# Kernel tuning notes

Hardware: AMD Instinct MI355X
Metric: run time of the kernel (lower is better)

## Reference

```python
import math
import jax, jax.numpy as jnp
import numpy as np

S = 2048   # padded sequence length (both src and tgt)
B = 8      # batch
D = 512    # d_embed
K = 64     # num_neighbors


def setup_inputs() -> dict:
    key = jax.random.key(0)
    ks = jax.random.split(key, 12)
    f32 = jnp.float32
    src_feats = jax.random.normal(ks[0], (S, B, D), f32)
    tgt_feats = jax.random.normal(ks[1], (S, B, D), f32)
    src_xyz = jax.random.normal(ks[2], (S, B, 3), f32)
    tgt_xyz = jax.random.normal(ks[3], (S, B, 3), f32)
    # lengths in [S - S//8, S] so every row has plenty of valid keys (>= K)
    src_lens = S - jax.random.randint(ks[4], (B,), 0, S // 8)
    tgt_lens = S - jax.random.randint(ks[5], (B,), 0, S // 8)
    scale = 1.0 / math.sqrt(D)
    Wq = jax.random.normal(ks[6], (D, D), f32) * scale
    bq = jnp.zeros((D,), f32)
    Wk = jax.random.normal(ks[7], (D, D), f32) * scale
    bk = jnp.zeros((D,), f32)
    Wc = jax.random.normal(ks[8], (1, D), f32) * scale
    bc = jnp.zeros((1,), f32)
    return dict(src_feats_padded=src_feats, tgt_feats_padded=tgt_feats,
                src_xyz_padded=src_xyz, tgt_xyz_padded=tgt_xyz,
                src_lens=src_lens, tgt_lens=tgt_lens,
                Wq=Wq, bq=bq, Wk=Wk, bk=bk, Wc=Wc, bc=bc)


def _simple_attention(query, key, value, key_padding_mask, Wq, bq, Wk, bk, num_neighbors):
    # query: (Q,B,D), key: (S,B,D), value: (S,B,E), key_padding_mask: (B,S) True=pad
    d = query.shape[-1]
    q = (query @ Wq.T + bq) / math.sqrt(d)          # (Q,B,D)
    k = key @ Wk.T + bk                              # (S,B,D)
    attn = jnp.einsum('qbd,sbd->bqs', q, k)          # (B,Q,S)
    attn = attn + jnp.where(key_padding_mask, -jnp.inf, 0.0)[:, None, :]
    if num_neighbors > 0:
        # Faithful to torch's `neighbor_mask[:, :, haha] = 0` (advanced indexing):
        # the UNION of top-k column indices over all (b,q) rows is unmasked for
        # every row; all other columns get -inf.
        idx = jax.lax.top_k(attn, num_neighbors)[1]              # (B,Q,K)
        col_mask = jnp.full((attn.shape[-1],), -jnp.inf, attn.dtype)
        col_mask = col_mask.at[idx.reshape(-1)].set(0.0)         # (S,)
        attn = attn + col_mask[None, None, :]
    attn = jax.nn.softmax(attn, axis=-1)
    return jnp.einsum('bqs,sbe->qbe', attn, value)   # (Q,B,E)


def _forward(src_feats, tgt_feats, src_xyz, tgt_xyz, src_lens, tgt_lens,
             Wq, bq, Wk, bk, Wc, bc):
    n_src, b = src_feats.shape[0], src_feats.shape[1]
    n_tgt = tgt_feats.shape[0]
    src_kpm = jnp.arange(n_src)[None, :] >= src_lens[:, None]   # (B,N_src)
    tgt_kpm = jnp.arange(n_tgt)[None, :] >= tgt_lens[:, None]   # (B,N_tgt)
    src_corr = _simple_attention(src_feats, tgt_feats, tgt_xyz, tgt_kpm,
                                 Wq, bq, Wk, bk, K)             # (N_src,B,3)
    tgt_corr = _simple_attention(tgt_feats, src_feats, src_xyz, src_kpm,
                                 Wq, bq, Wk, bk, K)             # (N_tgt,B,3)
    src_overlap = src_feats @ Wc.T + bc                          # (N_src,B,1)
    tgt_overlap = tgt_feats @ Wc.T + bc                          # (N_tgt,B,1)
    return src_corr, tgt_corr, src_overlap, tgt_overlap


def reference(src_feats_padded, tgt_feats_padded, src_xyz_padded, tgt_xyz_padded,
              src_lens, tgt_lens, Wq, bq, Wk, bk, Wc, bc):
    return _forward(src_feats_padded, tgt_feats_padded, src_xyz_padded,
                    tgt_xyz_padded, src_lens, tgt_lens, Wq, bq, Wk, bk, Wc, bc)
```

## Files before the change

kernel.cpp:

```cpp
#include <hip/hip_runtime.h>

typedef __attribute__((ext_vector_type(8))) short short8;
typedef __attribute__((ext_vector_type(4))) short s16x4;
typedef __attribute__((ext_vector_type(4))) float f32x4;

#define SEQ 2048
#define BAT 8
#define DIM 512
#define RSQRT_D 0.044194173824159216f

__device__ __forceinline__ unsigned short f2bf(float x) {
  union { float f; unsigned u; } v; v.f = x;
  unsigned r = (v.u + 0x7FFFu + ((v.u >> 16) & 1u)) >> 16;
  return (unsigned short)r;
}

__device__ __forceinline__ unsigned char f2fp8(float x) {
  return (unsigned char)(__builtin_amdgcn_cvt_pk_fp8_f32(x, x, 0, false) & 0xFF);
}

__device__ __forceinline__ void gload_lds16(const void* g, void* lds_base) {
  __builtin_amdgcn_global_load_lds(
      (const __attribute__((address_space(1))) unsigned int*)g,
      (__attribute__((address_space(3))) unsigned int*)lds_base,
      16, 0, 0);
}

__device__ __forceinline__ f32x4 mfma_pv(s16x4 a, s16x4 b, f32x4 c) {
  asm("v_mfma_f32_16x16x16_bf16 %0, %1, %2, %0" : "+v"(c) : "v"(a), "v"(b));
  return c;
}

__global__ __launch_bounds__(256) void k_pack(
    const float* __restrict__ src, const float* __restrict__ tgt,
    const float* __restrict__ Wc, const float* __restrict__ bc,
    const float* __restrict__ sxyz, const float* __restrict__ txyz,
    const float* __restrict__ Wq, const float* __restrict__ Wk,
    unsigned short* __restrict__ srcT, unsigned short* __restrict__ tgtT,
    float4* __restrict__ Vsrc, float4* __restrict__ Vtgt,
    unsigned short* __restrict__ Wqb, unsigned short* __restrict__ Wkb,
    float* __restrict__ out) {
  int which = blockIdx.y;
  if (blockIdx.x >= 4096) {
    int e = (blockIdx.x - 4096) * 256 + threadIdx.x;
    if (which == 0) {
      int wsel = e >> 15, j = e & 32767;
      const float* wp = (wsel ? Wk : Wq) + (size_t)j * 8;
      unsigned short* o = wsel ? Wkb : Wqb;
      float4 f0 = *(const float4*)wp, f1 = *(const float4*)(wp + 4);
      uint4 pk;
      pk.x = (unsigned)f2bf(f0.x) | ((unsigned)f2bf(f0.y) << 16);
      pk.y = (unsigned)f2bf(f0.z) | ((unsigned)f2bf(f0.w) << 16);
      pk.z = (unsigned)f2bf(f1.x) | ((unsigned)f2bf(f1.y) << 16);
      pk.w = (unsigned)f2bf(f1.z) | ((unsigned)f2bf(f1.w) << 16);
      *(uint4*)(o + (size_t)j * 8) = pk;
    } else if (e < 32768) {
      int wsel = e >> 14, id = e & 16383;
      int s = id >> 3, b = id & 7;
      const float* xyz = (wsel ? txyz : sxyz) + (size_t)id * 3;
      float4 v = make_float4(xyz[0], xyz[1], xyz[2], 0.f);
      (wsel ? Vtgt : Vsrc)[b * SEQ + s] = v;
    }
    return;
  }
  int w = threadIdx.x >> 6, lane = threadIdx.x & 63;
  int row = blockIdx.x * 4 + w;
  const float* in = (which ? tgt : src) + (size_t)row * DIM;
  unsigned short* T = which ? tgtT : srcT;
  int s = row >> 3, b = row & 7;

  const float4* in4 = (const float4*)in;
  float4 f0 = in4[lane * 2], f1 = in4[lane * 2 + 1];

  uint4 pk;
  pk.x = (unsigned)f2bf(f0.x) | ((unsigned)f2bf(f0.y) << 16);
  pk.y = (unsigned)f2bf(f0.z) | ((unsigned)f2bf(f0.w) << 16);
  pk.z = (unsigned)f2bf(f1.x) | ((unsigned)f2bf(f1.y) << 16);
  pk.w = (unsigned)f2bf(f1.z) | ((unsigned)f2bf(f1.w) << 16);
  *(uint4*)(T + ((size_t)(b * SEQ + s) * DIM + lane * 8)) = pk;

  const float4* wc4 = (const float4*)Wc;
  float4 w0 = wc4[lane * 2], w1 = wc4[lane * 2 + 1];
  float d = f0.x * w0.x + f0.y * w0.y + f0.z * w0.z + f0.w * w0.w +
            f1.x * w1.x + f1.y * w1.y + f1.z * w1.z + f1.w * w1.w;
  for (int o = 32; o; o >>= 1) d += __shfl_xor(d, o);
  if (lane == 0) {
    int base = which ? (SEQ * BAT * 6 + SEQ * BAT) : (SEQ * BAT * 6);
    out[base + row] = d + bc[0];
  }
}

__global__ __launch_bounds__(256) void k_proj(
    const unsigned short* __restrict__ srcT, const unsigned short* __restrict__ tgtT,
    const unsigned short* __restrict__ Wqb, const unsigned short* __restrict__ Wkb,
    const float* __restrict__ bq, const float* __restrict__ bk,
    unsigned char* __restrict__ Qsrc, unsigned char* __restrict__ Ktgt,
    unsigned char* __restrict__ Qtgt, unsigned char* __restrict__ Ksrc) {
  __shared__ __align__(16) char at[16384];
  __shared__ __align__(16) char bt[16384];
  int id = blockIdx.x;
  int x = id & 7, t = id >> 3;
  int m = x * 16 + (t >> 4);
  int inner = t & 15;
  int n = inner & 3, z = inner >> 2;
  bool isQ = (z == 0 || z == 2);
  const unsigned short* A = (z == 0 || z == 3) ? srcT : tgtT;
  const unsigned short* W = isQ ? Wqb : Wkb;
  const float* bias = isQ ? bq : bk;
  unsigned char* O = z == 0 ? Qsrc : z == 1 ? Ktgt : z == 2 ? Qtgt : Ksrc;

  int m0 = m * 128, n0 = n * 128;
  int tid = threadIdx.x, w = tid >> 6, lane = tid & 63;
  int ln = lane & 15, quad = lane >> 4;
  int moff = (w & 1) * 64, noff = (w >> 1) * 64;

  f32x4 acc[4][4];
  f32x4 zero = {0.f, 0.f, 0.f, 0.f};
  for (int mi = 0; mi < 4; ++mi)
    for (int ni = 0; ni < 4; ++ni) acc[mi][ni] = zero;

  for (int kb = 0; kb < DIM; kb += 64) {
    #pragma unroll
    for (int it = 0; it < 4; ++it) {
      int rbase = w * 32 + it * 8;
      int r = rbase + (lane >> 3);
      int c = (lane & 7) ^ (r & 7);
      gload_lds16(A + ((size_t)(m0 + r) * DIM + kb + c * 8), &at[rbase * 128]);
      gload_lds16(W + ((size_t)(n0 + r) * DIM + kb + c * 8), &bt[rbase * 128]);
    }
    __syncthreads();
    #pragma unroll
    for (int ks = 0; ks < 2; ++ks) {
      short8 afr[4], bfr[4];
      #pragma unroll
      for (int mi = 0; mi < 4; ++mi) {
        int r = moff + mi * 16 + ln;
        int p = (ks * 4 + quad) ^ (r & 7);
        afr[mi] = *(const short8*)(&at[r * 128 + p * 16]);
      }
      #pragma unroll
      for (int ni = 0; ni < 4; ++ni) {
        int r = noff + ni * 16 + ln;
        int p = (ks * 4 + quad) ^ (r & 7);
        bfr[ni] = *(const short8*)(&bt[r * 128 + p * 16]);
      }
      #pragma unroll
      for (int mi = 0; mi < 4; ++mi)
        #pragma unroll
        for (int ni = 0; ni < 4; ++ni)
          acc[mi][ni] = __builtin_amdgcn_mfma_f32_16x16x32_bf16(afr[mi], bfr[ni], acc[mi][ni], 0, 0, 0);
    }
    __syncthreads();
  }

  for (int ni = 0; ni < 4; ++ni) {
    int n_g = n0 + noff + ni * 16 + ln;
    float bv = bias[n_g];
    for (int mi = 0; mi < 4; ++mi) {
      int m_g = m0 + moff + mi * 16 + quad * 4;
      for (int r = 0; r < 4; ++r) {
        float v = acc[mi][ni][r] + bv;
        int row = m_g + r;
        size_t pos;
        if (isQ) pos = (size_t)row * DIM + n_g;
        else     pos = (size_t)row * DIM + ((((n_g >> 3) ^ (row & 15)) << 3) | (n_g & 7));
        O[pos] = f2fp8(v);
      }
    }
  }
}

__global__ __launch_bounds__(256) void k_attn(
    const unsigned char* __restrict__ Qsrc, const unsigned char* __restrict__ Ktgt,
    const unsigned char* __restrict__ Qtgt, const unsigned char* __restrict__ Ksrc,
    const float4* __restrict__ Vsrc, const float4* __restrict__ Vtgt,
    const int* __restrict__ src_lens, const int* __restrict__ tgt_lens,
    float4* __restrict__ part) {
  __shared__ __align__(16) char klds[16384];
  __shared__ __align__(16) char vaug[4096];
  int id = blockIdx.x;
  int x = id & 7, j = id >> 3;
  int group = (j >> 7) * 8 + x;
  int dir = group >> 3, b = group & 7;
  int inner = j & 127;
  int chunk = inner >> 5, qb = inner & 31;

  const unsigned char* Q = dir ? Qtgt : Qsrc;
  const unsigned char* K = dir ? Ksrc : Ktgt;
  const float4* V = dir ? Vsrc : Vtgt;
  int len = (dir ? src_lens : tgt_lens)[b];
  int k0g = chunk * 512;
  int kend = min(len, k0g + 512);
  int nblk = (kend - k0g + 31) >> 5;

  int tid = threadIdx.x, w = tid >> 6, lane = tid & 63;
  int ln = lane & 15, quad = lane >> 4;
  int q0 = qb * 64 + w * 16;

  if (tid < 128) {
    int rem = kend - k0g;
    const float4* vsrc = V + b * SEQ + k0g + tid * 4;
    float c[4][4];
    #pragma unroll
    for (int jj = 0; jj < 4; ++jj) {
      float4 vv = vsrc[jj];
      bool val = (tid * 4 + jj) < rem;
      c[0][jj] = val ? 1.f : 0.f;
      c[1][jj] = val ? vv.x : 0.f;
      c[2][jj] = val ? vv.y : 0.f;
      c[3][jj] = val ? vv.z : 0.f;
    }
    uint4 w0, w1;
    w0.x = (unsigned)f2bf(c[0][0]) | ((unsigned)f2bf(c[0][1]) << 16);
    w0.y = (unsigned)f2bf(c[0][2]) | ((unsigned)f2bf(c[0][3]) << 16);
    w0.z = (unsigned)f2bf(c[1][0]) | ((unsigned)f2bf(c[1][1]) << 16);
    w0.w = (unsigned)f2bf(c[1][2]) | ((unsigned)f2bf(c[1][3]) << 16);
    w1.x = (unsigned)f2bf(c[2][0]) | ((unsigned)f2bf(c[2][1]) << 16);
    w1.y = (unsigned)f2bf(c[2][2]) | ((unsigned)f2bf(c[2][3]) << 16);
    w1.z = (unsigned)f2bf(c[3][0]) | ((unsigned)f2bf(c[3][1]) << 16);
    w1.w = (unsigned)f2bf(c[3][2]) | ((unsigned)f2bf(c[3][3]) << 16);
    *(uint4*)(vaug + tid * 32) = w0;
    *(uint4*)(vaug + tid * 32 + 16) = w1;
  }

  long af[16];
  {
    const unsigned char* qrow = Q + (size_t)(b * SEQ + q0 + ln) * DIM + quad * 8;
    #pragma unroll
    for (int kk = 0; kk < 16; ++kk)
      af[kk] = *(const long*)(qrow + kk * 32);
  }

  f32x4 accPV = {0.f, 0.f, 0.f, 0.f};
  const unsigned char* kchunk = K + (size_t)(b * SEQ + k0g) * DIM;

  for (int kb = 0; kb < nblk; ++kb) {
    const unsigned char* kbase = kchunk + (size_t)kb * 32 * DIM;
    #pragma unroll
    for (int it = 0; it < 4; ++it) {
      int rp = w * 4 + it;
      gload_lds16(kbase + rp * 1024 + lane * 16, &klds[rp * 1024]);
    }
    __syncthreads();

    const char* krow0 = klds + ln * DIM;
    const char* krow1 = krow0 + 16 * DIM;

    f32x4 acc0 = {0.f, 0.f, 0.f, 0.f}, acc1 = {0.f, 0.f, 0.f, 0.f};
    __builtin_amdgcn_s_setprio(1);
    #pragma unroll
    for (int kk = 0; kk < 16; ++kk) {
      int pos = (((kk * 4 + quad) ^ ln) << 3);
      long b0 = *(const long*)(krow0 + pos);
      long b1 = *(const long*)(krow1 + pos);
      acc0 = __builtin_amdgcn_mfma_f32_16x16x32_fp8_fp8(b0, af[kk], acc0, 0, 0, 0);
      acc1 = __builtin_amdgcn_mfma_f32_16x16x32_fp8_fp8(b1, af[kk], acc1, 0, 0, 0);
    }
    __builtin_amdgcn_s_setprio(0);

    unsigned u00, u01, u10, u11;
    {
      float p0 = __expf(acc0[0] * RSQRT_D), p1 = __expf(acc0[1] * RSQRT_D);
      float p2 = __expf(acc0[2] * RSQRT_D), p3 = __expf(acc0[3] * RSQRT_D);
      asm("v_cvt_pk_bf16_f32 %0, %1, %2" : "=v"(u00) : "v"(p0), "v"(p1));
      asm("v_cvt_pk_bf16_f32 %0, %1, %2" : "=v"(u01) : "v"(p2), "v"(p3));
      float r0 = __expf(acc1[0] * RSQRT_D), r1 = __expf(acc1[1] * RSQRT_D);
      float r2 = __expf(acc1[2] * RSQRT_D), r3 = __expf(acc1[3] * RSQRT_D);
      asm("v_cvt_pk_bf16_f32 %0, %1, %2" : "=v"(u10) : "v"(r0), "v"(r1));
      asm("v_cvt_pk_bf16_f32 %0, %1, %2" : "=v"(u11) : "v"(r2), "v"(r3));
    }
    union U { unsigned u[2]; s16x4 s; };
    U pb0; pb0.u[0] = u00; pb0.u[1] = u01;
    U pb1; pb1.u[0] = u10; pb1.u[1] = u11;

    int voff = kb * 256 + quad * 32 + (ln & 3) * 8;
    s16x4 va0 = *(const s16x4*)(vaug + voff);
    s16x4 va1 = *(const s16x4*)(vaug + voff + 128);
    accPV = mfma_pv(va0, pb0.s, accPV);
    accPV = mfma_pv(va1, pb1.s, accPV);

    __syncthreads();
  }

  if (quad == 0) {
    int q = q0 + ln;
    part[((size_t)(dir * BAT + b) * 4 + chunk) * SEQ + q] =
        make_float4(accPV[0], accPV[1], accPV[2], accPV[3]);
  }
}

__global__ __launch_bounds__(256) void k_attn_reduce(
    const float4* __restrict__ part, float* __restrict__ out) {
  int t = blockIdx.x * 256 + threadIdx.x;
  int dir = t >> 14, rem = t & 16383, b = rem >> 11, q = rem & 2047;
  size_t base = ((size_t)(dir * BAT + b) * 4) * SEQ + q;
  float4 s0 = part[base];
  float4 s1 = part[base + SEQ];
  float4 s2 = part[base + 2 * SEQ];
  float4 s3 = part[base + 3 * SEQ];
  float inv = 1.f / (s0.x + s1.x + s2.x + s3.x);
  float* ob = out + (size_t)dir * (SEQ * BAT * 3) + ((size_t)q * BAT + b) * 3;
  ob[0] = (s0.y + s1.y + s2.y + s3.y) * inv;
  ob[1] = (s0.z + s1.z + s2.z + s3.z) * inv;
  ob[2] = (s0.w + s1.w + s2.w + s3.w) * inv;
}

extern "C" void kernel_launch(void* const* d_in, const int* in_sizes, int n_in,
                              void* d_out, int out_size, void* d_ws, size_t ws_size,
                              hipStream_t stream) {
  const float* src  = (const float*)d_in[0];
  const float* tgt  = (const float*)d_in[1];
  const float* sxyz = (const float*)d_in[2];
  const float* txyz = (const float*)d_in[3];
  const int* slens  = (const int*)d_in[4];
  const int* tlens  = (const int*)d_in[5];
  const float* Wq   = (const float*)d_in[6];
  const float* bq   = (const float*)d_in[7];
  const float* Wk   = (const float*)d_in[8];
  const float* bk   = (const float*)d_in[9];
  const float* Wc   = (const float*)d_in[10];
  const float* bc   = (const float*)d_in[11];
  float* out = (float*)d_out;

  char* ws = (char*)d_ws;
  size_t off = 0;
  auto carve = [&](size_t bytes) -> char* {
    char* p = ws + off;
    off += (bytes + 255) & ~(size_t)255;
    return p;
  };
  const size_t FEAT_BF  = (size_t)BAT * SEQ * DIM * 2;
  const size_t FEAT_FP8 = (size_t)BAT * SEQ * DIM;
  unsigned short* srcT = (unsigned short*)carve(FEAT_BF);
  unsigned short* tgtT = (unsigned short*)carve(FEAT_BF);
  unsigned char* Qsrc = (unsigned char*)carve(FEAT_FP8);
  unsigned char* Ktgt = (unsigned char*)carve(FEAT_FP8);
  unsigned char* Qtgt = (unsigned char*)carve(FEAT_FP8);
  unsigned char* Ksrc = (unsigned char*)carve(FEAT_FP8);
  unsigned short* Wqb  = (unsigned short*)carve((size_t)DIM * DIM * 2);
  unsigned short* Wkb  = (unsigned short*)carve((size_t)DIM * DIM * 2);
  float4* Vsrc = (float4*)carve((size_t)BAT * SEQ * 16);
  float4* Vtgt = (float4*)carve((size_t)BAT * SEQ * 16);
  float4* part = (float4*)srcT;

  k_pack<<<dim3(4352, 2), 256, 0, stream>>>(src, tgt, Wc, bc, sxyz, txyz, Wq, Wk,
                                            srcT, tgtT, Vsrc, Vtgt, Wqb, Wkb, out);
  k_proj<<<dim3(2048), 256, 0, stream>>>(srcT, tgtT, Wqb, Wkb, bq, bk,
                                         Qsrc, Ktgt, Qtgt, Ksrc);
  k_attn<<<dim3(2048), 256, 0, stream>>>(Qsrc, Ktgt, Qtgt, Ksrc, Vsrc, Vtgt,
                                         slens, tlens, part);
  k_attn_reduce<<<dim3(128), 256, 0, stream>>>(part, out);
}
```

Baseline: 238.4 us.

## Process two query tiles per block to double K-tile reuse in attention

```diff
diff --git a/kernel.cpp b/kernel.cpp
--- a/kernel.cpp
+++ b/kernel.cpp
@@ -180,10 +180,10 @@
   __shared__ __align__(16) char vaug[4096];
   int id = blockIdx.x;
   int x = id & 7, j = id >> 3;
-  int group = (j >> 7) * 8 + x;
+  int group = (j >> 6) * 8 + x;
   int dir = group >> 3, b = group & 7;
-  int inner = j & 127;
-  int chunk = inner >> 5, qb = inner & 31;
+  int inner = j & 63;
+  int chunk = inner >> 4, qb = inner & 15;
 
   const unsigned char* Q = dir ? Qtgt : Qsrc;
   const unsigned char* K = dir ? Ksrc : Ktgt;
@@ -195,7 +195,7 @@
 
   int tid = threadIdx.x, w = tid >> 6, lane = tid & 63;
   int ln = lane & 15, quad = lane >> 4;
-  int q0 = qb * 64 + w * 16;
+  int q0 = qb * 128 + w * 16;
 
   if (tid < 128) {
     int rem = kend - k0g;
@@ -223,15 +223,19 @@
     *(uint4*)(vaug + tid * 32 + 16) = w1;
   }
 
-  long af[16];
+  long af[16], ag[16];
   {
-    const unsigned char* qrow = Q + (size_t)(b * SEQ + q0 + ln) * DIM + quad * 8;
-    #pragma unroll
-    for (int kk = 0; kk < 16; ++kk)
-      af[kk] = *(const long*)(qrow + kk * 32);
-  }
-
-  f32x4 accPV = {0.f, 0.f, 0.f, 0.f};
+    const unsigned char* qrowA = Q + (size_t)(b * SEQ + q0 + ln) * DIM + quad * 8;
+    const unsigned char* qrowB = qrowA + (size_t)64 * DIM;
+    #pragma unroll
+    for (int kk = 0; kk < 16; ++kk) {
+      af[kk] = *(const long*)(qrowA + kk * 32);
+      ag[kk] = *(const long*)(qrowB + kk * 32);
+    }
+  }
+
+  f32x4 accPV0 = {0.f, 0.f, 0.f, 0.f};
+  f32x4 accPV1 = {0.f, 0.f, 0.f, 0.f};
   const unsigned char* kchunk = K + (size_t)(b * SEQ + k0g) * DIM;
 
   for (int kb = 0; kb < nblk; ++kb) {
@@ -247,6 +251,7 @@
     const char* krow1 = krow0 + 16 * DIM;
 
     f32x4 acc0 = {0.f, 0.f, 0.f, 0.f}, acc1 = {0.f, 0.f, 0.f, 0.f};
+    f32x4 acc2 = {0.f, 0.f, 0.f, 0.f}, acc3 = {0.f, 0.f, 0.f, 0.f};
     __builtin_amdgcn_s_setprio(1);
     #pragma unroll
     for (int kk = 0; kk < 16; ++kk) {
@@ -255,37 +260,49 @@
       long b1 = *(const long*)(krow1 + pos);
       acc0 = __builtin_amdgcn_mfma_f32_16x16x32_fp8_fp8(b0, af[kk], acc0, 0, 0, 0);
       acc1 = __builtin_amdgcn_mfma_f32_16x16x32_fp8_fp8(b1, af[kk], acc1, 0, 0, 0);
+      acc2 = __builtin_amdgcn_mfma_f32_16x16x32_fp8_fp8(b0, ag[kk], acc2, 0, 0, 0);
+      acc3 = __builtin_amdgcn_mfma_f32_16x16x32_fp8_fp8(b1, ag[kk], acc3, 0, 0, 0);
     }
     __builtin_amdgcn_s_setprio(0);
 
-    unsigned u00, u01, u10, u11;
+    union U { unsigned u[2]; s16x4 s; };
+    U pA0, pA1, pB0, pB1;
     {
       float p0 = __expf(acc0[0] * RSQRT_D), p1 = __expf(acc0[1] * RSQRT_D);
       float p2 = __expf(acc0[2] * RSQRT_D), p3 = __expf(acc0[3] * RSQRT_D);
-      asm("v_cvt_pk_bf16_f32 %0, %1, %2" : "=v"(u00) : "v"(p0), "v"(p1));
-      asm("v_cvt_pk_bf16_f32 %0, %1, %2" : "=v"(u01) : "v"(p2), "v"(p3));
+      asm("v_cvt_pk_bf16_f32 %0, %1, %2" : "=v"(pA0.u[0]) : "v"(p0), "v"(p1));
+      asm("v_cvt_pk_bf16_f32 %0, %1, %2" : "=v"(pA0.u[1]) : "v"(p2), "v"(p3));
       float r0 = __expf(acc1[0] * RSQRT_D), r1 = __expf(acc1[1] * RSQRT_D);
       float r2 = __expf(acc1[2] * RSQRT_D), r3 = __expf(acc1[3] * RSQRT_D);
-      asm("v_cvt_pk_bf16_f32 %0, %1, %2" : "=v"(u10) : "v"(r0), "v"(r1));
-      asm("v_cvt_pk_bf16_f32 %0, %1, %2" : "=v"(u11) : "v"(r2), "v"(r3));
-    }
-    union U { unsigned u[2]; s16x4 s; };
-    U pb0; pb0.u[0] = u00; pb0.u[1] = u01;
-    U pb1; pb1.u[0] = u10; pb1.u[1] = u11;
+      asm("v_cvt_pk_bf16_f32 %0, %1, %2" : "=v"(pA1.u[0]) : "v"(r0), "v"(r1));
+      asm("v_cvt_pk_bf16_f32 %0, %1, %2" : "=v"(pA1.u[1]) : "v"(r2), "v"(r3));
+      float s0 = __expf(acc2[0] * RSQRT_D), s1 = __expf(acc2[1] * RSQRT_D);
+      float s2 = __expf(acc2[2] * RSQRT_D), s3 = __expf(acc2[3] * RSQRT_D);
+      asm("v_cvt_pk_bf16_f32 %0, %1, %2" : "=v"(pB0.u[0]) : "v"(s0), "v"(s1));
+      asm("v_cvt_pk_bf16_f32 %0, %1, %2" : "=v"(pB0.u[1]) : "v"(s2), "v"(s3));
+      float t0 = __expf(acc3[0] * RSQRT_D), t1 = __expf(acc3[1] * RSQRT_D);
+      float t2 = __expf(acc3[2] * RSQRT_D), t3 = __expf(acc3[3] * RSQRT_D);
+      asm("v_cvt_pk_bf16_f32 %0, %1, %2" : "=v"(pB1.u[0]) : "v"(t0), "v"(t1));
+      asm("v_cvt_pk_bf16_f32 %0, %1, %2" : "=v"(pB1.u[1]) : "v"(t2), "v"(t3));
+    }
 
     int voff = kb * 256 + quad * 32 + (ln & 3) * 8;
     s16x4 va0 = *(const s16x4*)(vaug + voff);
     s16x4 va1 = *(const s16x4*)(vaug + voff + 128);
-    accPV = mfma_pv(va0, pb0.s, accPV);
-    accPV = mfma_pv(va1, pb1.s, accPV);
+    accPV0 = mfma_pv(va0, pA0.s, accPV0);
+    accPV0 = mfma_pv(va1, pA1.s, accPV0);
+    accPV1 = mfma_pv(va0, pB0.s, accPV1);
+    accPV1 = mfma_pv(va1, pB1.s, accPV1);
 
     __syncthreads();
   }
 
   if (quad == 0) {
-    int q = q0 + ln;
-    part[((size_t)(dir * BAT + b) * 4 + chunk) * SEQ + q] =
-        make_float4(accPV[0], accPV[1], accPV[2], accPV[3]);
+    size_t base = ((size_t)(dir * BAT + b) * 4 + chunk) * SEQ;
+    part[base + q0 + ln] =
+        make_float4(accPV0[0], accPV0[1], accPV0[2], accPV0[3]);
+    part[base + q0 + 64 + ln] =
+        make_float4(accPV1[0], accPV1[1], accPV1[2], accPV1[3]);
   }
 }
 
@@ -347,7 +364,7 @@
                                             srcT, tgtT, Vsrc, Vtgt, Wqb, Wkb, out);
   k_proj<<<dim3(2048), 256, 0, stream>>>(srcT, tgtT, Wqb, Wkb, bq, bk,
                                          Qsrc, Ktgt, Qtgt, Ksrc);
-  k_attn<<<dim3(2048), 256, 0, stream>>>(Qsrc, Ktgt, Qtgt, Ksrc, Vsrc, Vtgt,
+  k_attn<<<dim3(1024), 256, 0, stream>>>(Qsrc, Ktgt, Qtgt, Ksrc, Vsrc, Vtgt,
                                          slens, tlens, part);
   k_attn_reduce<<<dim3(128), 256, 0, stream>>>(part, out);
 }
```

Result: faster. 231.3 us (-3.0%).
